# Performance work log

Measured on AMD Instinct MI355X. Metric: run time of the kernel, lower is better.

## Reference

```python
import jax, jax.numpy as jnp
import numpy as np

EPS = 1e-5  # torch LayerNorm default

def _ln(x, w, b):
    mu = jnp.mean(x, axis=-1, keepdims=True)
    var = jnp.mean((x - mu) ** 2, axis=-1, keepdims=True)
    return (x - mu) * jax.lax.rsqrt(var + EPS) * w + b

def setup_inputs() -> dict:
    B, C, P, D = 256, 256, 256, 256  # broadcasting in final add requires B==P==C
    key = jax.random.key(0)
    ks = jax.random.split(key, 10)
    d_rsqrt = D ** -0.5
    return {
        "x": jax.random.normal(ks[0], (B, C), dtype=jnp.float32),
        "prev_cell_out": jax.random.normal(ks[1], (P, D), dtype=jnp.float32),
        "feature_emb_weight": jax.random.uniform(ks[2], (C, D), minval=-d_rsqrt, maxval=d_rsqrt),
        "feature_emb_bias": jax.random.uniform(ks[3], (1, C, D), minval=-d_rsqrt, maxval=d_rsqrt),
        "ln_emb_w": jnp.ones((D,), jnp.float32), "ln_emb_b": jnp.zeros((D,), jnp.float32),
        "ln_col_w": jnp.ones((D,), jnp.float32), "ln_col_b": jnp.zeros((D,), jnp.float32),
        "ln_prompt_w": jnp.ones((D,), jnp.float32), "ln_prompt_b": jnp.zeros((D,), jnp.float32),
        "dense_imp_w": jax.random.normal(ks[4], (D, 2 * D)) * (2 * D) ** -0.5,  # torch Linear weight [out,in]
        "dense_imp_b": jnp.zeros((D,), jnp.float32),
        "emb_column": jax.random.normal(ks[5], (C, D)) * 0.01,
        "emb_prompt": jax.random.normal(ks[6], (P, D)) * 0.01,
        "expand_weight": jax.random.normal(ks[7], (P, 1)),  # dense_expand.weight [n_prompts, 1]
        "expand_bias": jax.random.normal(ks[8], (P,)) * 0.01,
    }

def reference(x, prev_cell_out, feature_emb_weight, feature_emb_bias,
              ln_emb_w, ln_emb_b, ln_col_w, ln_col_b, ln_prompt_w, ln_prompt_b,
              dense_imp_w, dense_imp_b, emb_column, emb_prompt,
              expand_weight, expand_bias):
    # addcmul: bias + x[...,None] * weight -> [B, C, D]
    x_emb = _ln(jax.nn.relu(feature_emb_bias + x[..., None] * feature_emb_weight), ln_emb_w, ln_emb_b)
    # prompt path (unbatched): [P, 2D] -> [P, D]
    xp_in = jnp.concatenate([_ln(emb_prompt, ln_prompt_w, ln_prompt_b), prev_cell_out], axis=-1)
    x_prompt = xp_in @ dense_imp_w.T + dense_imp_b + emb_prompt
    x_col = _ln(emb_column, ln_col_w, ln_col_b)  # [C, D]
    mask = jax.nn.softmax(x_prompt @ x_col.T, axis=-1)  # [P, C]
    # einsum 'pc,bcd->bpd'
    x_out = jnp.einsum('pc,bcd->bpd', mask, x_emb)
    # 'pc,bcd,pa->bpd' with a==1 is the same contraction scaled per-prompt by expand_weight[p,0]
    x_out = x_out * (1.0 + expand_weight[:, 0])[None, :, None]
    # 'pc,p->pc' then unsqueeze(0).unsqueeze(-1): [1, P, C, 1]; broadcasts [B,P,D] -> [1,B,P,D]
    bias_term = (mask * expand_bias[:, None])[None, :, :, None]
    return x_out + bias_term  # [1, B, P, D] (B==P==C)
```

## Files before the change

kernel.cpp:

```cpp
#include <hip/hip_runtime.h>
#include <cstdint>

typedef _Float16 half8 __attribute__((ext_vector_type(8)));
typedef float f32x4 __attribute__((ext_vector_type(4)));

#define LN_EPS 1e-5f

__device__ __forceinline__ float dot4(float4 a, float4 b) {
  return a.x*b.x + a.y*b.y + a.z*b.z + a.w*b.w;
}

__global__ __launch_bounds__(256) void k_pre(
    const float* __restrict__ x, const float* __restrict__ few, const float* __restrict__ feb,
    const float* __restrict__ emb_pr, const float* __restrict__ lnp_w, const float* __restrict__ lnp_b,
    const float* __restrict__ prev, const float* __restrict__ W, const float* __restrict__ Wb,
    const float* __restrict__ emb_col, const float* __restrict__ lnc_w, const float* __restrict__ lnc_b,
    float2* __restrict__ stats2, float* __restrict__ mask_f32, _Float16* __restrict__ mask_f16)
{
  __shared__ __align__(16) struct {
    float xin[512];
    float xq[256];
    float sc[256];
    float wr1[4], wr2[4];
  } sm;

  int t = threadIdx.x, w = t >> 6, lane = t & 63;

  if (blockIdx.x >= 256) {
    int bid = blockIdx.x - 256;
    int b = bid >> 3;
    int cg = (bid & 7) * 4 + w;
    int c0 = cg * 8;
    float xv[8];
    #pragma unroll
    for (int j = 0; j < 8; ++j) xv[j] = x[b*256 + c0 + j];
    float s1[8], s2[8];
    #pragma unroll
    for (int j = 0; j < 8; ++j) { s1[j] = 0.f; s2[j] = 0.f; }
    #pragma unroll
    for (int j = 0; j < 8; ++j) {
      float4 fw = ((const float4*)few)[(c0+j)*64 + lane];
      float4 fb = ((const float4*)feb)[(c0+j)*64 + lane];
      float4 v;
      v.x = fmaxf(fb.x + xv[j]*fw.x, 0.f);
      v.y = fmaxf(fb.y + xv[j]*fw.y, 0.f);
      v.z = fmaxf(fb.z + xv[j]*fw.z, 0.f);
      v.w = fmaxf(fb.w + xv[j]*fw.w, 0.f);
      s1[j] += v.x + v.y + v.z + v.w;
      s2[j] += v.x*v.x + v.y*v.y + v.z*v.z + v.w*v.w;
    }
    #pragma unroll
    for (int o = 32; o > 0; o >>= 1) {
      #pragma unroll
      for (int j = 0; j < 8; ++j) { s1[j] += __shfl_xor(s1[j], o); s2[j] += __shfl_xor(s2[j], o); }
    }
    float mu[8], rs[8];
    #pragma unroll
    for (int j = 0; j < 8; ++j) {
      mu[j] = s1[j] * (1.0f/256.0f);
      float var = s2[j] * (1.0f/256.0f) - mu[j]*mu[j];
      rs[j] = rsqrtf(var + LN_EPS);
    }
    float muv = mu[0], rsv = rs[0];
    #pragma unroll
    for (int j = 1; j < 8; ++j) {
      muv = (lane == j) ? mu[j] : muv;
      rsv = (lane == j) ? rs[j] : rsv;
    }
    if (lane < 8) stats2[b*256 + c0 + lane] = make_float2(muv, rsv);
    return;
  }

  int p = blockIdx.x;
  int q = t & 3, g = t >> 2;

  {
    float4 v = ((const float4*)emb_pr)[p*64 + lane];
    float s1 = v.x + v.y + v.z + v.w;
    float s2 = v.x*v.x + v.y*v.y + v.z*v.z + v.w*v.w;
    #pragma unroll
    for (int o = 32; o > 0; o >>= 1) { s1 += __shfl_xor(s1, o); s2 += __shfl_xor(s2, o); }
    float mu = s1 * (1.0f/256.0f);
    float var = s2 * (1.0f/256.0f) - mu*mu;
    float rsv = rsqrtf(var + LN_EPS);
    float4 w4 = ((const float4*)lnp_w)[lane];
    float4 b4 = ((const float4*)lnp_b)[lane];
    float4 y;
    y.x = (v.x-mu)*rsv*w4.x + b4.x;  y.y = (v.y-mu)*rsv*w4.y + b4.y;
    y.z = (v.z-mu)*rsv*w4.z + b4.z;  y.w = (v.w-mu)*rsv*w4.w + b4.w;
    if (w == 0) {
      ((float4*)sm.xin)[lane] = y;
      ((float4*)sm.xin)[64 + lane] = ((const float4*)prev)[p*64 + lane];
    }
  }
  __syncthreads();

  {
    float acc[4] = {0.f, 0.f, 0.f, 0.f};
    #pragma unroll 4
    for (int j = 0; j < 32; ++j) {
      int k4 = j*4 + q;
      float4 xv = ((const float4*)sm.xin)[k4];
      #pragma unroll
      for (int pp = 0; pp < 4; ++pp) {
        int d = pp*64 + g;
        float4 wv = ((const float4*)W)[d*128 + k4];
        acc[pp] += dot4(wv, xv);
      }
    }
    #pragma unroll
    for (int pp = 0; pp < 4; ++pp) {
      acc[pp] += __shfl_xor(acc[pp], 1);
      acc[pp] += __shfl_xor(acc[pp], 2);
    }
    if (q == 0) {
      #pragma unroll
      for (int pp = 0; pp < 4; ++pp) {
        int d = pp*64 + g;
        sm.xq[d] = acc[pp] + Wb[d] + emb_pr[p*256 + d];
      }
    }
  }
  __syncthreads();

  {
    float s1[4] = {0,0,0,0}, s2[4] = {0,0,0,0};
    #pragma unroll 4
    for (int j = 0; j < 16; ++j) {
      int k4 = j*4 + q;
      #pragma unroll
      for (int pp = 0; pp < 4; ++pp) {
        float4 v = ((const float4*)emb_col)[(pp*64+g)*64 + k4];
        s1[pp] += v.x + v.y + v.z + v.w;
        s2[pp] += v.x*v.x + v.y*v.y + v.z*v.z + v.w*v.w;
      }
    }
    float mu[4], rs[4];
    #pragma unroll
    for (int pp = 0; pp < 4; ++pp) {
      s1[pp] += __shfl_xor(s1[pp], 1);  s1[pp] += __shfl_xor(s1[pp], 2);
      s2[pp] += __shfl_xor(s2[pp], 1);  s2[pp] += __shfl_xor(s2[pp], 2);
      mu[pp] = s1[pp] * (1.0f/256.0f);
      float var = s2[pp] * (1.0f/256.0f) - mu[pp]*mu[pp];
      rs[pp] = rsqrtf(var + LN_EPS);
    }
    float acc[4] = {0.f, 0.f, 0.f, 0.f};
    #pragma unroll 4
    for (int j = 0; j < 16; ++j) {
      int k4 = j*4 + q;
      float4 lw4 = ((const float4*)lnc_w)[k4];
      float4 lb4 = ((const float4*)lnc_b)[k4];
      float4 xv = ((const float4*)sm.xq)[k4];
      #pragma unroll
      for (int pp = 0; pp < 4; ++pp) {
        float4 v = ((const float4*)emb_col)[(pp*64+g)*64 + k4];
        float4 nc;
        nc.x = (v.x-mu[pp])*rs[pp]*lw4.x + lb4.x;
        nc.y = (v.y-mu[pp])*rs[pp]*lw4.y + lb4.y;
        nc.z = (v.z-mu[pp])*rs[pp]*lw4.z + lb4.z;
        nc.w = (v.w-mu[pp])*rs[pp]*lw4.w + lb4.w;
        acc[pp] += dot4(nc, xv);
      }
    }
    #pragma unroll
    for (int pp = 0; pp < 4; ++pp) {
      acc[pp] += __shfl_xor(acc[pp], 1);
      acc[pp] += __shfl_xor(acc[pp], 2);
    }
    if (q == 0) {
      #pragma unroll
      for (int pp = 0; pp < 4; ++pp) sm.sc[pp*64 + g] = acc[pp];
    }
  }
  __syncthreads();

  {
    float val = sm.sc[t];
    float m0 = val;
    #pragma unroll
    for (int o = 32; o > 0; o >>= 1) m0 = fmaxf(m0, __shfl_xor(m0, o));
    if (lane == 0) sm.wr1[w] = m0;
    __syncthreads();
    float M = fmaxf(fmaxf(sm.wr1[0], sm.wr1[1]), fmaxf(sm.wr1[2], sm.wr1[3]));
    float e = expf(val - M);
    float s = e;
    #pragma unroll
    for (int o = 32; o > 0; o >>= 1) s += __shfl_xor(s, o);
    if (lane == 0) sm.wr2[w] = s;
    __syncthreads();
    float S = sm.wr2[0] + sm.wr2[1] + sm.wr2[2] + sm.wr2[3];
    float mv = e / S;
    mask_f32[p*256 + t] = mv;
    mask_f16[p*256 + t] = (_Float16)mv;
  }
}

__global__ __launch_bounds__(256) void k_main(
    const float* __restrict__ x, const float* __restrict__ few, const float* __restrict__ feb,
    const float* __restrict__ ln_emb_w, const float* __restrict__ ln_emb_b,
    const float2* __restrict__ stats2,
    const _Float16* __restrict__ mask_f16, const float* __restrict__ mask_f32,
    const float* __restrict__ ew, const float* __restrict__ eb,
    float* __restrict__ out)
{
  __shared__ __align__(16) _Float16 Bs[4 * 8 * 64 * 8];
  __shared__ float xrow[256];
  __shared__ __align__(8) float2 srow[256];

  const int t = threadIdx.x, w = t >> 6, lane = t & 63;
  const int lm = lane & 15, quad = lane >> 4;
  const int b  = blockIdx.x >> 2;
  const int ds = (blockIdx.x & 3) * 64;
  const int dl = t & 63;
  const int d  = ds + dl;

  half8 mf0[2][4], mf1[2][4];
  #pragma unroll
  for (int ks = 0; ks < 2; ++ks)
    #pragma unroll
    for (int nt = 0; nt < 4; ++nt)
      mf0[ks][nt] = *(const half8*)(mask_f16 + (size_t)(w*64 + nt*16 + lm)*256 + ks*32 + quad*8);

  xrow[t] = x[b*256 + t];
  srow[t] = stats2[b*256 + t];
  const float lwv = ln_emb_w[d];
  const float lbv = ln_emb_b[d];

  f32x4 acc[4][4];
  #pragma unroll
  for (int i = 0; i < 4; ++i)
    #pragma unroll
    for (int j = 0; j < 4; ++j)
      acc[i][j] = (f32x4){0.f, 0.f, 0.f, 0.f};

  __syncthreads();

  #pragma unroll
  for (int kb = 0; kb < 4; ++kb) {
    float fwv[16], fbv[16];
    #pragma unroll
    for (int j = 0; j < 16; ++j) {
      int cl = kb*64 + w*16 + j;
      fwv[j] = few[cl*256 + d];
      fbv[j] = feb[cl*256 + d];
    }
    half8 h0, h1;
    #pragma unroll
    for (int j = 0; j < 16; ++j) {
      int cl = kb*64 + w*16 + j;
      float2 st = srow[cl];
      float v = fmaxf(fbv[j] + xrow[cl]*fwv[j], 0.f);
      _Float16 hh = (_Float16)((v - st.x) * st.y * lwv + lbv);
      if (j < 8) h0[j] = hh; else h1[j-8] = hh;
    }
    *(half8*)(&Bs[((kb*8 + w*2 + 0)*64 + dl)*8]) = h0;
    *(half8*)(&Bs[((kb*8 + w*2 + 1)*64 + dl)*8]) = h1;
  }
  __syncthreads();

#define MFMA_KB(KB, MFC, MFN, DO_PRE)                                           \
  {                                                                             \
    if (DO_PRE) {                                                               \
      _Pragma("unroll") for (int ks = 0; ks < 2; ++ks)                          \
        _Pragma("unroll") for (int nt = 0; nt < 4; ++nt)                        \
          MFN[ks][nt] = *(const half8*)(mask_f16 +                              \
              (size_t)(w*64 + nt*16 + lm)*256 + ((KB)+1)*64 + ks*32 + quad*8);  \
    }                                                                           \
    _Pragma("unroll") for (int ks = 0; ks < 2; ++ks) {                          \
      half8 xf[4];                                                              \
      _Pragma("unroll") for (int mt = 0; mt < 4; ++mt)                          \
        xf[mt] = *(const half8*)(&Bs[(((KB)*8 + ks*4 + quad)*64 + mt*16 + lm)*8]); \
      _Pragma("unroll") for (int mt = 0; mt < 4; ++mt)                          \
        _Pragma("unroll") for (int nt = 0; nt < 4; ++nt)                        \
          acc[mt][nt] = __builtin_amdgcn_mfma_f32_16x16x32_f16(                 \
              xf[mt], MFC[ks][nt], acc[mt][nt], 0, 0, 0);                       \
    }                                                                           \
  }

  MFMA_KB(0, mf0, mf1, 1)
  MFMA_KB(1, mf1, mf0, 1)
  MFMA_KB(2, mf0, mf1, 1)
  MFMA_KB(3, mf1, mf0, 0)
#undef MFMA_KB

  const float ebv = eb[b];
  float sp[4], tb[4];
  #pragma unroll
  for (int nt = 0; nt < 4; ++nt) {
    int p = w*64 + nt*16 + lm;
    sp[nt] = 1.0f + ew[p];
    tb[nt] = mask_f32[b*256 + p] * ebv;
  }
  #pragma unroll
  for (int mt = 0; mt < 4; ++mt) {
    #pragma unroll
    for (int nt = 0; nt < 4; ++nt) {
      int p = w*64 + nt*16 + lm;
      int dd = ds + mt*16 + quad*4;
      f32x4 o = acc[mt][nt] * sp[nt] + tb[nt];
      *(f32x4*)(out + ((size_t)b << 16) + ((size_t)p << 8) + dd) = o;
    }
  }
}

extern "C" void kernel_launch(void* const* d_in, const int* in_sizes, int n_in,
                              void* d_out, int out_size, void* d_ws, size_t ws_size,
                              hipStream_t stream) {
  const float* x        = (const float*)d_in[0];
  const float* prev     = (const float*)d_in[1];
  const float* few      = (const float*)d_in[2];
  const float* feb      = (const float*)d_in[3];
  const float* ln_emb_w = (const float*)d_in[4];
  const float* ln_emb_b = (const float*)d_in[5];
  const float* ln_col_w = (const float*)d_in[6];
  const float* ln_col_b = (const float*)d_in[7];
  const float* ln_pr_w  = (const float*)d_in[8];
  const float* ln_pr_b  = (const float*)d_in[9];
  const float* dimp_w   = (const float*)d_in[10];
  const float* dimp_b   = (const float*)d_in[11];
  const float* emb_col  = (const float*)d_in[12];
  const float* emb_pr   = (const float*)d_in[13];
  const float* ew       = (const float*)d_in[14];
  const float* eb       = (const float*)d_in[15];
  float* out = (float*)d_out;

  char* wsb = (char*)d_ws;
  float2*   ws_stats  = (float2*)(wsb);
  float*    ws_mask   = (float*)(wsb + 524288);
  _Float16* ws_mask_h = (_Float16*)(wsb + 786432);

  k_pre<<<dim3(256 + 2048), dim3(256), 0, stream>>>(
      x, few, feb,
      emb_pr, ln_pr_w, ln_pr_b, prev, dimp_w, dimp_b,
      emb_col, ln_col_w, ln_col_b,
      ws_stats, ws_mask, ws_mask_h);
  k_main<<<dim3(1024), dim3(256), 0, stream>>>(
      x, few, feb, ln_emb_w, ln_emb_b,
      ws_stats, ws_mask_h, ws_mask, ew, eb, out);
}
```

Baseline: 146.6 us.

## Split fused embed+GEMM kernel into producer writing fp16 x_emb and separate MFMA GEMM

The fused main kernel, which built the layer-normed embedding tile in shared memory and then ran MFMA, is split in two when the workspace is large enough. A producer kernel writes the fp16 embedding in MFMA-fragment layout to global memory, and a GEMM kernel reads it directly without shared memory or barriers. This aims to remove the LDS staging and synchronisation stalls and let each kernel get better occupancy. The cost is an extra 32 MB global write and read plus one more launch. The fused kernel stays as a fallback when the workspace is too small.

```diff
diff --git a/kernel.cpp b/kernel.cpp
--- a/kernel.cpp
+++ b/kernel.cpp
@@ -195,7 +195,114 @@
   }
 }
 
-__global__ __launch_bounds__(256) void k_main(
+__global__ __launch_bounds__(256) void k_prod(
+    const float* __restrict__ x, const float* __restrict__ few, const float* __restrict__ feb,
+    const float* __restrict__ ln_emb_w, const float* __restrict__ ln_emb_b,
+    const float2* __restrict__ stats2, _Float16* __restrict__ xemb)
+{
+  __shared__ float xrow[256];
+  __shared__ __align__(8) float2 srow[256];
+
+  const int t = threadIdx.x, w = t >> 6;
+  const int b  = blockIdx.x >> 2;
+  const int ds = (blockIdx.x & 3) * 64;
+  const int dl = t & 63;
+  const int d  = ds + dl;
+
+  xrow[t] = x[b*256 + t];
+  srow[t] = stats2[b*256 + t];
+  const float lwv = ln_emb_w[d];
+  const float lbv = ln_emb_b[d];
+  __syncthreads();
+
+  _Float16* xg = xemb + (size_t)blockIdx.x * 16384;
+
+  #pragma unroll
+  for (int kb = 0; kb < 4; ++kb) {
+    float fwv[16], fbv[16];
+    #pragma unroll
+    for (int j = 0; j < 16; ++j) {
+      int cl = kb*64 + w*16 + j;
+      fwv[j] = few[cl*256 + d];
+      fbv[j] = feb[cl*256 + d];
+    }
+    half8 h0, h1;
+    #pragma unroll
+    for (int j = 0; j < 16; ++j) {
+      int cl = kb*64 + w*16 + j;
+      float2 st = srow[cl];
+      float v = fmaxf(fbv[j] + xrow[cl]*fwv[j], 0.f);
+      _Float16 hh = (_Float16)((v - st.x) * st.y * lwv + lbv);
+      if (j < 8) h0[j] = hh; else h1[j-8] = hh;
+    }
+    *(half8*)(xg + (size_t)((kb*8 + w*2 + 0)*64 + dl)*8) = h0;
+    *(half8*)(xg + (size_t)((kb*8 + w*2 + 1)*64 + dl)*8) = h1;
+  }
+}
+
+__global__ __launch_bounds__(256) void k_gemm(
+    const _Float16* __restrict__ xemb,
+    const _Float16* __restrict__ mask_f16, const float* __restrict__ mask_f32,
+    const float* __restrict__ ew, const float* __restrict__ eb,
+    float* __restrict__ out)
+{
+  const int t = threadIdx.x, w = t >> 6, lane = t & 63;
+  const int lm = lane & 15, quad = lane >> 4;
+  const int b  = blockIdx.x >> 2;
+  const int ds = (blockIdx.x & 3) * 64;
+
+  const _Float16* xg = xemb + (size_t)blockIdx.x * 16384;
+
+  f32x4 acc[4][4];
+  #pragma unroll
+  for (int i = 0; i < 4; ++i)
+    #pragma unroll
+    for (int j = 0; j < 4; ++j)
+      acc[i][j] = (f32x4){0.f, 0.f, 0.f, 0.f};
+
+  #pragma unroll
+  for (int kb = 0; kb < 4; ++kb) {
+    half8 mf[2][4];
+    #pragma unroll
+    for (int ks = 0; ks < 2; ++ks)
+      #pragma unroll
+      for (int nt = 0; nt < 4; ++nt)
+        mf[ks][nt] = *(const half8*)(mask_f16 + (size_t)(w*64 + nt*16 + lm)*256 + kb*64 + ks*32 + quad*8);
+    #pragma unroll
+    for (int ks = 0; ks < 2; ++ks) {
+      half8 xf[4];
+      #pragma unroll
+      for (int mt = 0; mt < 4; ++mt)
+        xf[mt] = *(const half8*)(xg + (size_t)((kb*8 + ks*4 + quad)*64 + mt*16 + lm)*8);
+      #pragma unroll
+      for (int mt = 0; mt < 4; ++mt)
+        #pragma unroll
+        for (int nt = 0; nt < 4; ++nt)
+          acc[mt][nt] = __builtin_amdgcn_mfma_f32_16x16x32_f16(xf[mt], mf[ks][nt], acc[mt][nt], 0, 0, 0);
+    }
+  }
+
+  const float ebv = eb[b];
+  float sp[4], tb[4];
+  #pragma unroll
+  for (int nt = 0; nt < 4; ++nt) {
+    int p = w*64 + nt*16 + lm;
+    sp[nt] = 1.0f + ew[p];
+    tb[nt] = mask_f32[b*256 + p] * ebv;
+  }
+  #pragma unroll
+  for (int mt = 0; mt < 4; ++mt) {
+    #pragma unroll
+    for (int nt = 0; nt < 4; ++nt) {
+      int p = w*64 + nt*16 + lm;
+      int dd = ds + mt*16 + quad*4;
+      f32x4 o = acc[mt][nt] * sp[nt] + tb[nt];
+      *(f32x4*)(out + ((size_t)b << 16) + ((size_t)p << 8) + dd) = o;
+    }
+  }
+}
+
+__global__ __launch_bounds__(256) void k_main_fused(
     const float* __restrict__ x, const float* __restrict__ few, const float* __restrict__ feb,
     const float* __restrict__ ln_emb_w, const float* __restrict__ ln_emb_b,
     const float2* __restrict__ stats2,
@@ -328,13 +435,24 @@
   float2*   ws_stats  = (float2*)(wsb);
   float*    ws_mask   = (float*)(wsb + 524288);
   _Float16* ws_mask_h = (_Float16*)(wsb + 786432);
+  _Float16* ws_xemb   = (_Float16*)(wsb + 917504);
+
+  const size_t need = 917504 + (size_t)1024 * 16384 * sizeof(_Float16);
 
   k_pre<<<dim3(256 + 2048), dim3(256), 0, stream>>>(
       x, few, feb,
       emb_pr, ln_pr_w, ln_pr_b, prev, dimp_w, dimp_b,
       emb_col, ln_col_w, ln_col_b,
       ws_stats, ws_mask, ws_mask_h);
-  k_main<<<dim3(1024), dim3(256), 0, stream>>>(
-      x, few, feb, ln_emb_w, ln_emb_b,
-      ws_stats, ws_mask_h, ws_mask, ew, eb, out);
-}
+
+  if (ws_size >= need) {
+    k_prod<<<dim3(1024), dim3(256), 0, stream>>>(
+        x, few, feb, ln_emb_w, ln_emb_b, ws_stats, ws_xemb);
+    k_gemm<<<dim3(1024), dim3(256), 0, stream>>>(
+        ws_xemb, ws_mask_h, ws_mask, ew, eb, out);
+  } else {
+    k_main_fused<<<dim3(1024), dim3(256), 0, stream>>>(
+        x, few, feb, ln_emb_w, ln_emb_b,
+        ws_stats, ws_mask_h, ws_mask, ew, eb, out);
+  }
+}
```

After: 159.5 us. +8.8%, slower.
